# Optimization experiments

Measured on AMD Instinct MI355X. Metric: run time of the kernel, lower is better.

Reference implementation:

```python
import jax, jax.numpy as jnp
import numpy as np

K = 6                      # max_displacement / pad_size
WIN = 2 * K + 1            # displacement window side
D = WIN * WIN              # number of affinity channels (169)


def setup_inputs() -> dict:
    key = jax.random.key(0)
    k1, k2 = jax.random.split(key)
    aff = jax.random.normal(k1, (4, D, 192, 192), dtype=jnp.float32)
    input2 = jax.random.normal(k2, (4, 64, 192, 192), dtype=jnp.float32)
    return {"aff": aff, "input2": input2}


def reference(aff, input2):
    # output[b,c,y,x] = sum_{dy,dx in [-k,k]} aff[b, idx(dy,dx), y, x]
    #                   * input2_zeropad[b, c, y+dy, x+dx]
    # Scanned over the (2k+1)^2 displacements to avoid materializing the
    # [B, D, C, H, W] cost-volume intermediate.
    B, C, H, W = input2.shape
    Dn = aff.shape[1]
    win = int(round(Dn ** 0.5))
    k = (win - 1) // 2
    padded = jnp.pad(input2, ((0, 0), (0, 0), (k, k), (k, k)))  # [B,C,H+2k,W+2k]
    aff_t = jnp.transpose(aff, (1, 0, 2, 3))  # [D,B,H,W]
    ds = jnp.arange(Dn)

    def body(acc, xs):
        d, a = xs                      # a: [B,H,W]
        dy = d // win                  # 0..2k (offset into padded rows)
        dx = d % win                   # 0..2k (offset into padded cols)
        patch = jax.lax.dynamic_slice(padded, (0, 0, dy, dx), (B, C, H, W))
        return acc + a[:, None, :, :] * patch, None

    out, _ = jax.lax.scan(body, jnp.zeros_like(input2), (ds, aff_t))
    return out
```

## Files before the change

### kernel.cpp

```cpp
#include <hip/hip_runtime.h>


#define KD   6
#define WIN  13
#define ND   169
#define NB   4
#define NC   64
#define NH   192
#define NW   192
#define XH   96
#define PITCHW 68
#define NTH  192

typedef _Float16 half2v __attribute__((ext_vector_type(2)));

static __device__ __forceinline__ half2v h2(unsigned u) {
    return __builtin_bit_cast(half2v, u);
}
static __device__ __forceinline__ unsigned pk(float a, float b) {
    return __builtin_bit_cast(unsigned, __builtin_amdgcn_cvt_pkrtz(a, b));
}

#if __has_builtin(__builtin_amdgcn_fdot2)
#define FDOT2(a, b, c) __builtin_amdgcn_fdot2((a), (b), (c), false)
#else
static __device__ __forceinline__ float fdot2_fb(half2v a, half2v b, float c) {
    return fmaf((float)a.x, (float)b.x, fmaf((float)a.y, (float)b.y, c));
}
#define FDOT2(a, b, c) fdot2_fb((a), (b), (c))
#endif

__global__ __launch_bounds__(NTH)
__attribute__((amdgpu_waves_per_eu(2, 4)))
void mxassemble(const float* __restrict__ aff,
                const float* __restrict__ in2,
                float* __restrict__ out) {
    __shared__ unsigned ldsw[NC * PITCHW];

    const int y    = blockIdx.x;
    const int half = blockIdx.y;
    const int b    = blockIdx.z;
    const int t    = threadIdx.x;
    const int l    = t & 63;
    const int wv   = t >> 6;
    const int cg   = l & 7;
    const int xs   = l >> 3;
    const int X0   = half * XH;
    const int x0   = X0 + wv * 32 + xs * 4;

    {
        const int w0 = (half == 0) ? 0 : 52;
        for (int i = t; i < NC * 2; i += NTH) {
            const int c = i >> 1;
            const int q = i & 1;
            *(uint2*)&ldsw[c * PITCHW + w0 + 2 * q] = make_uint2(0u, 0u);
        }
    }

    float acc[8][4];
#pragma unroll
    for (int i = 0; i < 8; ++i)
#pragma unroll
        for (int j = 0; j < 4; ++j) acc[i][j] = 0.f;

    const float* in2_b = in2 + (size_t)b * NC * NH * NW;
    const float* aff_p = aff + (size_t)b * ND * NH * NW + (size_t)y * NW;

    for (int dy = 0; dy < WIN; ++dy) {
        const int r = y + dy - KD;
        const bool valid = (r >= 0) && (r < NH);

        __syncthreads();

        unsigned Ap[6][4];
        unsigned Al[4];
        if (valid) {
            const float* ap = aff_p + (size_t)(dy * WIN) * NH * NW + x0;
            float4 Af[13];
#pragma unroll
            for (int dx = 0; dx < WIN; ++dx)
                Af[dx] = *(const float4*)&ap[(size_t)dx * NH * NW];

            for (int ii = t; ii < NC * 28; ii += NTH) {
                const int c  = ii / 28;
                const int q  = ii - c * 28;
                const int xg = X0 - 8 + 4 * q;
                if (xg >= 0 && xg < NW) {
                    const float4 v =
                        *(const float4*)&in2_b[((size_t)c * NH + r) * NW + xg];
                    uint2 w;
                    w.x = pk(v.x, v.y);
                    w.y = pk(v.z, v.w);
                    *(uint2*)&ldsw[c * PITCHW + 2 * q] = w;
                }
            }

#pragma unroll
            for (int m = 0; m < 6; ++m) {
                Ap[m][0] = pk(Af[2*m].x, Af[2*m+1].x);
                Ap[m][1] = pk(Af[2*m].y, Af[2*m+1].y);
                Ap[m][2] = pk(Af[2*m].z, Af[2*m+1].z);
                Ap[m][3] = pk(Af[2*m].w, Af[2*m+1].w);
            }
            Al[0] = pk(Af[12].x, 0.f);
            Al[1] = pk(Af[12].y, 0.f);
            Al[2] = pk(Af[12].z, 0.f);
            Al[3] = pk(Af[12].w, 0.f);
        }
        __syncthreads();
        if (!valid) continue;

#pragma unroll
        for (int i = 0; i < 8; ++i) {
            const int c = cg + 8 * i;
            const unsigned* wp = &ldsw[c * PITCHW + ((x0 - X0) >> 1)];
            const uint2 t0 = *(const uint2*)&wp[0];
            const uint2 t1 = *(const uint2*)&wp[2];
            const uint2 t2 = *(const uint2*)&wp[4];
            const uint2 t3 = *(const uint2*)&wp[6];
            const uint2 t4 = *(const uint2*)&wp[8];
            const unsigned P1 = t0.y, P2 = t1.x, P3 = t1.y, P4 = t2.x;
            const unsigned P5 = t2.y, P6 = t3.x, P7 = t3.y, P8 = t4.x;
            const unsigned P9 = t4.y;
            const unsigned S1 = (P1 >> 16) | (P2 << 16);
            const unsigned S2 = (P2 >> 16) | (P3 << 16);
            const unsigned S3 = (P3 >> 16) | (P4 << 16);
            const unsigned S4 = (P4 >> 16) | (P5 << 16);
            const unsigned S5 = (P5 >> 16) | (P6 << 16);
            const unsigned S6 = (P6 >> 16) | (P7 << 16);
            const unsigned S7 = (P7 >> 16) | (P8 << 16);
            const unsigned S8 = (P8 >> 16) | (P9 << 16);

            float a0 = acc[i][0], a1 = acc[i][1], a2 = acc[i][2], a3 = acc[i][3];
            a0 = FDOT2(h2(Ap[0][0]), h2(P1), a0);
            a0 = FDOT2(h2(Ap[1][0]), h2(P2), a0);
            a0 = FDOT2(h2(Ap[2][0]), h2(P3), a0);
            a0 = FDOT2(h2(Ap[3][0]), h2(P4), a0);
            a0 = FDOT2(h2(Ap[4][0]), h2(P5), a0);
            a0 = FDOT2(h2(Ap[5][0]), h2(P6), a0);
            a0 = FDOT2(h2(Al[0]),    h2(P7), a0);
            a1 = FDOT2(h2(Ap[0][1]), h2(S1), a1);
            a1 = FDOT2(h2(Ap[1][1]), h2(S2), a1);
            a1 = FDOT2(h2(Ap[2][1]), h2(S3), a1);
            a1 = FDOT2(h2(Ap[3][1]), h2(S4), a1);
            a1 = FDOT2(h2(Ap[4][1]), h2(S5), a1);
            a1 = FDOT2(h2(Ap[5][1]), h2(S6), a1);
            a1 = FDOT2(h2(Al[1]),    h2(S7), a1);
            a2 = FDOT2(h2(Ap[0][2]), h2(P2), a2);
            a2 = FDOT2(h2(Ap[1][2]), h2(P3), a2);
            a2 = FDOT2(h2(Ap[2][2]), h2(P4), a2);
            a2 = FDOT2(h2(Ap[3][2]), h2(P5), a2);
            a2 = FDOT2(h2(Ap[4][2]), h2(P6), a2);
            a2 = FDOT2(h2(Ap[5][2]), h2(P7), a2);
            a2 = FDOT2(h2(Al[2]),    h2(P8), a2);
            a3 = FDOT2(h2(Ap[0][3]), h2(S2), a3);
            a3 = FDOT2(h2(Ap[1][3]), h2(S3), a3);
            a3 = FDOT2(h2(Ap[2][3]), h2(S4), a3);
            a3 = FDOT2(h2(Ap[3][3]), h2(S5), a3);
            a3 = FDOT2(h2(Ap[4][3]), h2(S6), a3);
            a3 = FDOT2(h2(Ap[5][3]), h2(S7), a3);
            a3 = FDOT2(h2(Al[3]),    h2(S8), a3);
            acc[i][0] = a0; acc[i][1] = a1; acc[i][2] = a2; acc[i][3] = a3;
        }
    }

    float* ob = out + (((size_t)(b * NC + cg) * NH) + y) * NW + x0;
#pragma unroll
    for (int i = 0; i < 8; ++i) {
        *(float4*)&ob[(size_t)(8 * i) * NH * NW] =
            make_float4(acc[i][0], acc[i][1], acc[i][2], acc[i][3]);
    }
}

extern "C" void kernel_launch(void* const* d_in, const int* in_sizes, int n_in,
                              void* d_out, int out_size, void* d_ws, size_t ws_size,
                              hipStream_t stream) {
    const float* aff = (const float*)d_in[0];
    const float* in2 = (const float*)d_in[1];
    float* outp = (float*)d_out;
    dim3 grid(NH, NW / XH, NB);
    dim3 block(NTH);
    hipLaunchKernelGGL(mxassemble, grid, block, 0, stream, aff, in2, outp);
}
```

Measured before the change: 308.3 us.

## Compute two output rows per block with double-buffered LDS row staging

Each block now produces two adjacent output rows over a 64-wide x tile. It streams 14 input rows through a double-buffered LDS and reuses each staged row for both output rows. Global loads for the next row and its affinity are issued before the current row's dot products, so load latency can overlap compute and there is one barrier per row. The grid is remapped with an interleaved block index, and the thread/channel split changes to 16 channel groups over 256 threads. Risks are higher register pressure from two accumulator sets and two packed-affinity sets, plus more halo traffic per output from the narrower tile.

```diff
diff --git a/kernel.cpp b/kernel.cpp
--- a/kernel.cpp
+++ b/kernel.cpp
@@ -8,9 +8,10 @@
 #define NC   64
 #define NH   192
 #define NW   192
-#define XH   96
-#define PITCHW 68
-#define NTH  192
+#define XH   64
+#define PITCHW 42
+#define BUFW (NC * PITCHW)
+#define NTH  256
 
 typedef _Float16 half2v __attribute__((ext_vector_type(2)));
 
@@ -30,145 +31,204 @@
 #define FDOT2(a, b, c) fdot2_fb((a), (b), (c))
 #endif
 
-__global__ __launch_bounds__(NTH)
-__attribute__((amdgpu_waves_per_eu(2, 4)))
+static __device__ __forceinline__ void aff_issue(const float* __restrict__ ap,
+                                                 float4 (&Af)[13]) {
+#pragma unroll
+    for (int dx = 0; dx < WIN; ++dx)
+        Af[dx] = *(const float4*)&ap[(size_t)dx * (NH * NW)];
+}
+
+static __device__ __forceinline__ void aff_pack(const float4 (&Af)[13],
+                                                unsigned (&P)[7][4]) {
+#pragma unroll
+    for (int m = 0; m < 6; ++m) {
+        P[m][0] = pk(Af[2*m].x, Af[2*m+1].x);
+        P[m][1] = pk(Af[2*m].y, Af[2*m+1].y);
+        P[m][2] = pk(Af[2*m].z, Af[2*m+1].z);
+        P[m][3] = pk(Af[2*m].w, Af[2*m+1].w);
+    }
+    P[6][0] = pk(Af[12].x, 0.f);
+    P[6][1] = pk(Af[12].y, 0.f);
+    P[6][2] = pk(Af[12].z, 0.f);
+    P[6][3] = pk(Af[12].w, 0.f);
+}
+
+static __device__ __forceinline__ void pass_y(const unsigned* __restrict__ wpb,
+                                              const unsigned (&P)[7][4],
+                                              float (&acc)[4][4]) {
+#pragma unroll
+    for (int i = 0; i < 4; ++i) {
+        const unsigned* wp = wpb + i * (16 * PITCHW);
+        const uint2 t0 = *(const uint2*)&wp[0];
+        const uint2 t1 = *(const uint2*)&wp[2];
+        const uint2 t2 = *(const uint2*)&wp[4];
+        const uint2 t3 = *(const uint2*)&wp[6];
+        const uint2 t4 = *(const uint2*)&wp[8];
+        const unsigned P1 = t0.y, P2 = t1.x, P3 = t1.y, P4 = t2.x;
+        const unsigned P5 = t2.y, P6 = t3.x, P7 = t3.y, P8 = t4.x;
+        const unsigned P9 = t4.y;
+        const unsigned S1 = (P1 >> 16) | (P2 << 16);
+        const unsigned S2 = (P2 >> 16) | (P3 << 16);
+        const unsigned S3 = (P3 >> 16) | (P4 << 16);
+        const unsigned S4 = (P4 >> 16) | (P5 << 16);
+        const unsigned S5 = (P5 >> 16) | (P6 << 16);
+        const unsigned S6 = (P6 >> 16) | (P7 << 16);
+        const unsigned S7 = (P7 >> 16) | (P8 << 16);
+        const unsigned S8 = (P8 >> 16) | (P9 << 16);
+
+        float a0 = acc[i][0], a1 = acc[i][1], a2 = acc[i][2], a3 = acc[i][3];
+        a0 = FDOT2(h2(P[0][0]), h2(P1), a0);
+        a0 = FDOT2(h2(P[1][0]), h2(P2), a0);
+        a0 = FDOT2(h2(P[2][0]), h2(P3), a0);
+        a0 = FDOT2(h2(P[3][0]), h2(P4), a0);
+        a0 = FDOT2(h2(P[4][0]), h2(P5), a0);
+        a0 = FDOT2(h2(P[5][0]), h2(P6), a0);
+        a0 = FDOT2(h2(P[6][0]), h2(P7), a0);
+        a1 = FDOT2(h2(P[0][1]), h2(S1), a1);
+        a1 = FDOT2(h2(P[1][1]), h2(S2), a1);
+        a1 = FDOT2(h2(P[2][1]), h2(S3), a1);
+        a1 = FDOT2(h2(P[3][1]), h2(S4), a1);
+        a1 = FDOT2(h2(P[4][1]), h2(S5), a1);
+        a1 = FDOT2(h2(P[5][1]), h2(S6), a1);
+        a1 = FDOT2(h2(P[6][1]), h2(S7), a1);
+        a2 = FDOT2(h2(P[0][2]), h2(P2), a2);
+        a2 = FDOT2(h2(P[1][2]), h2(P3), a2);
+        a2 = FDOT2(h2(P[2][2]), h2(P4), a2);
+        a2 = FDOT2(h2(P[3][2]), h2(P5), a2);
+        a2 = FDOT2(h2(P[4][2]), h2(P6), a2);
+        a2 = FDOT2(h2(P[5][2]), h2(P7), a2);
+        a2 = FDOT2(h2(P[6][2]), h2(P8), a2);
+        a3 = FDOT2(h2(P[0][3]), h2(S2), a3);
+        a3 = FDOT2(h2(P[1][3]), h2(S3), a3);
+        a3 = FDOT2(h2(P[2][3]), h2(S4), a3);
+        a3 = FDOT2(h2(P[3][3]), h2(S5), a3);
+        a3 = FDOT2(h2(P[4][3]), h2(S6), a3);
+        a3 = FDOT2(h2(P[5][3]), h2(S7), a3);
+        a3 = FDOT2(h2(P[6][3]), h2(S8), a3);
+        acc[i][0] = a0; acc[i][1] = a1; acc[i][2] = a2; acc[i][3] = a3;
+    }
+}
+
+__global__ __launch_bounds__(NTH, 2)
 void mxassemble(const float* __restrict__ aff,
                 const float* __restrict__ in2,
                 float* __restrict__ out) {
-    __shared__ unsigned ldsw[NC * PITCHW];
-
-    const int y    = blockIdx.x;
-    const int half = blockIdx.y;
-    const int b    = blockIdx.z;
+    __shared__ unsigned ldsw[2 * BUFW];
+
+    const int bx = blockIdx.x;
+    const int g  = bx & 7;
+    const int k  = bx >> 3;
+    const int b  = k / 12;
+    const int by = 12 * g + (k - 12 * b);
+    const int y0 = 2 * by;
+    const int xb = blockIdx.y;
+    const int X0 = xb * XH;
+
     const int t    = threadIdx.x;
     const int l    = t & 63;
     const int wv   = t >> 6;
-    const int cg   = l & 7;
-    const int xs   = l >> 3;
-    const int X0   = half * XH;
-    const int x0   = X0 + wv * 32 + xs * 4;
-
-    {
-        const int w0 = (half == 0) ? 0 : 52;
-        for (int i = t; i < NC * 2; i += NTH) {
-            const int c = i >> 1;
-            const int q = i & 1;
-            *(uint2*)&ldsw[c * PITCHW + w0 + 2 * q] = make_uint2(0u, 0u);
+    const int cg   = l & 15;
+    const int xs   = l >> 4;
+    const int slot = wv * 4 + xs;
+    const int x0   = X0 + slot * 4;
+
+    if (xb != 1) {
+        const int w0 = (xb == 0) ? 0 : 36;
+        if (t < NC * 2) {
+            const int c = t >> 1, qq = t & 1;
+            *(uint2*)&ldsw[c * PITCHW + w0 + 2 * qq]        = make_uint2(0u, 0u);
+            *(uint2*)&ldsw[BUFW + c * PITCHW + w0 + 2 * qq] = make_uint2(0u, 0u);
         }
     }
 
-    float acc[8][4];
-#pragma unroll
-    for (int i = 0; i < 8; ++i)
-#pragma unroll
-        for (int j = 0; j < 4; ++j) acc[i][j] = 0.f;
-
-    const float* in2_b = in2 + (size_t)b * NC * NH * NW;
-    const float* aff_p = aff + (size_t)b * ND * NH * NW + (size_t)y * NW;
-
-    for (int dy = 0; dy < WIN; ++dy) {
-        const int r = y + dy - KD;
-        const bool valid = (r >= 0) && (r < NH);
-
+    int wadr[5], goff[5];
+#pragma unroll
+    for (int s = 0; s < 5; ++s) {
+        const int ii = t + NTH * s;
+        const int c  = ii / 20;
+        const int q  = ii - 20 * c;
+        const int xg = X0 - 8 + 4 * q;
+        const bool ok = (xg >= 0) && (xg < NW);
+        wadr[s] = ok ? (c * PITCHW + 2 * q) : -1;
+        goff[s] = c * (NH * NW) + xg;
+    }
+
+    float acc0[4][4], acc1[4][4];
+#pragma unroll
+    for (int i = 0; i < 4; ++i)
+#pragma unroll
+        for (int j = 0; j < 4; ++j) { acc0[i][j] = 0.f; acc1[i][j] = 0.f; }
+
+    const float* in2_b  = in2 + (size_t)b * NC * NH * NW;
+    const float* aff_y0 = aff + (size_t)b * ND * NH * NW + (size_t)y0 * NW + x0;
+    const float* aff_y1 = aff_y0 + NW;
+    const int wbase = cg * PITCHW + 2 * slot;
+
+    float4 Af[13];
+    unsigned PA[7][4], PB[7][4];
+
+    aff_issue(aff_y0, Af);
+    if (y0 - KD >= 0) {
+        const float* p = in2_b + (size_t)(y0 - KD) * NW;
+        float4 Sv[5];
+#pragma unroll
+        for (int s = 0; s < 5; ++s)
+            if (wadr[s] >= 0) Sv[s] = *(const float4*)&p[goff[s]];
+#pragma unroll
+        for (int s = 0; s < 5; ++s)
+            if (wadr[s] >= 0) {
+                uint2 w; w.x = pk(Sv[s].x, Sv[s].y); w.y = pk(Sv[s].z, Sv[s].w);
+                *(uint2*)&ldsw[wadr[s]] = w;
+            }
+    }
+    aff_pack(Af, PA);
+    __syncthreads();
+
+    const float* apB = aff_y1;
+    const float* apA = aff_y0 + (size_t)(WIN * NH * NW);
+
+    for (int rr = 0; rr < 14; ++rr) {
+        const int r = y0 - KD + rr;
+        const bool rowvalid = (r >= 0) && (r < NH);
+        const int rn = r + 1;
+        const bool stage_next = (rr < 13) && (rn >= 0) && (rn < NH);
+        unsigned* curw = ldsw + ((rr & 1) ? BUFW : 0);
+        unsigned* nxtw = ldsw + ((rr & 1) ? 0 : BUFW);
+
+        if (rr < 13) aff_issue(apB, Af);
+        float4 Sv[5];
+        if (stage_next) {
+            const float* p = in2_b + (size_t)rn * NW;
+#pragma unroll
+            for (int s = 0; s < 5; ++s)
+                if (wadr[s] >= 0) Sv[s] = *(const float4*)&p[goff[s]];
+        }
+        if (rowvalid && rr >= 1) pass_y(curw + wbase, PB, acc1);
+        if (rr < 13) aff_pack(Af, PB);
+        if (stage_next) {
+#pragma unroll
+            for (int s = 0; s < 5; ++s)
+                if (wadr[s] >= 0) {
+                    uint2 w; w.x = pk(Sv[s].x, Sv[s].y); w.y = pk(Sv[s].z, Sv[s].w);
+                    *(uint2*)&nxtw[wadr[s]] = w;
+                }
+        }
+        if (rr < 12) aff_issue(apA, Af);
+        if (rowvalid && rr <= 12) pass_y(curw + wbase, PA, acc0);
+        if (rr < 12) aff_pack(Af, PA);
+
+        apB += (size_t)(WIN * NH * NW);
+        apA += (size_t)(WIN * NH * NW);
         __syncthreads();
-
-        unsigned Ap[6][4];
-        unsigned Al[4];
-        if (valid) {
-            const float* ap = aff_p + (size_t)(dy * WIN) * NH * NW + x0;
-            float4 Af[13];
-#pragma unroll
-            for (int dx = 0; dx < WIN; ++dx)
-                Af[dx] = *(const float4*)&ap[(size_t)dx * NH * NW];
-
-            for (int ii = t; ii < NC * 28; ii += NTH) {
-                const int c  = ii / 28;
-                const int q  = ii - c * 28;
-                const int xg = X0 - 8 + 4 * q;
-                if (xg >= 0 && xg < NW) {
-                    const float4 v =
-                        *(const float4*)&in2_b[((size_t)c * NH + r) * NW + xg];
-                    uint2 w;
-                    w.x = pk(v.x, v.y);
-                    w.y = pk(v.z, v.w);
-                    *(uint2*)&ldsw[c * PITCHW + 2 * q] = w;
-                }
-            }
-
-#pragma unroll
-            for (int m = 0; m < 6; ++m) {
-                Ap[m][0] = pk(Af[2*m].x, Af[2*m+1].x);
-                Ap[m][1] = pk(Af[2*m].y, Af[2*m+1].y);
-                Ap[m][2] = pk(Af[2*m].z, Af[2*m+1].z);
-                Ap[m][3] = pk(Af[2*m].w, Af[2*m+1].w);
-            }
-            Al[0] = pk(Af[12].x, 0.f);
-            Al[1] = pk(Af[12].y, 0.f);
-            Al[2] = pk(Af[12].z, 0.f);
-            Al[3] = pk(Af[12].w, 0.f);
-        }
-        __syncthreads();
-        if (!valid) continue;
-
-#pragma unroll
-        for (int i = 0; i < 8; ++i) {
-            const int c = cg + 8 * i;
-            const unsigned* wp = &ldsw[c * PITCHW + ((x0 - X0) >> 1)];
-            const uint2 t0 = *(const uint2*)&wp[0];
-            const uint2 t1 = *(const uint2*)&wp[2];
-            const uint2 t2 = *(const uint2*)&wp[4];
-            const uint2 t3 = *(const uint2*)&wp[6];
-            const uint2 t4 = *(const uint2*)&wp[8];
-            const unsigned P1 = t0.y, P2 = t1.x, P3 = t1.y, P4 = t2.x;
-            const unsigned P5 = t2.y, P6 = t3.x, P7 = t3.y, P8 = t4.x;
-            const unsigned P9 = t4.y;
-            const unsigned S1 = (P1 >> 16) | (P2 << 16);
-            const unsigned S2 = (P2 >> 16) | (P3 << 16);
-            const unsigned S3 = (P3 >> 16) | (P4 << 16);
-            const unsigned S4 = (P4 >> 16) | (P5 << 16);
-            const unsigned S5 = (P5 >> 16) | (P6 << 16);
-            const unsigned S6 = (P6 >> 16) | (P7 << 16);
-            const unsigned S7 = (P7 >> 16) | (P8 << 16);
-            const unsigned S8 = (P8 >> 16) | (P9 << 16);
-
-            float a0 = acc[i][0], a1 = acc[i][1], a2 = acc[i][2], a3 = acc[i][3];
-            a0 = FDOT2(h2(Ap[0][0]), h2(P1), a0);
-            a0 = FDOT2(h2(Ap[1][0]), h2(P2), a0);
-            a0 = FDOT2(h2(Ap[2][0]), h2(P3), a0);
-            a0 = FDOT2(h2(Ap[3][0]), h2(P4), a0);
-            a0 = FDOT2(h2(Ap[4][0]), h2(P5), a0);
-            a0 = FDOT2(h2(Ap[5][0]), h2(P6), a0);
-            a0 = FDOT2(h2(Al[0]),    h2(P7), a0);
-            a1 = FDOT2(h2(Ap[0][1]), h2(S1), a1);
-            a1 = FDOT2(h2(Ap[1][1]), h2(S2), a1);
-            a1 = FDOT2(h2(Ap[2][1]), h2(S3), a1);
-            a1 = FDOT2(h2(Ap[3][1]), h2(S4), a1);
-            a1 = FDOT2(h2(Ap[4][1]), h2(S5), a1);
-            a1 = FDOT2(h2(Ap[5][1]), h2(S6), a1);
-            a1 = FDOT2(h2(Al[1]),    h2(S7), a1);
-            a2 = FDOT2(h2(Ap[0][2]), h2(P2), a2);
-            a2 = FDOT2(h2(Ap[1][2]), h2(P3), a2);
-            a2 = FDOT2(h2(Ap[2][2]), h2(P4), a2);
-            a2 = FDOT2(h2(Ap[3][2]), h2(P5), a2);
-            a2 = FDOT2(h2(Ap[4][2]), h2(P6), a2);
-            a2 = FDOT2(h2(Ap[5][2]), h2(P7), a2);
-            a2 = FDOT2(h2(Al[2]),    h2(P8), a2);
-            a3 = FDOT2(h2(Ap[0][3]), h2(S2), a3);
-            a3 = FDOT2(h2(Ap[1][3]), h2(S3), a3);
-            a3 = FDOT2(h2(Ap[2][3]), h2(S4), a3);
-            a3 = FDOT2(h2(Ap[3][3]), h2(S5), a3);
-            a3 = FDOT2(h2(Ap[4][3]), h2(S6), a3);
-            a3 = FDOT2(h2(Ap[5][3]), h2(S7), a3);
-            a3 = FDOT2(h2(Al[3]),    h2(S8), a3);
-            acc[i][0] = a0; acc[i][1] = a1; acc[i][2] = a2; acc[i][3] = a3;
-        }
-    }
-
-    float* ob = out + (((size_t)(b * NC + cg) * NH) + y) * NW + x0;
-#pragma unroll
-    for (int i = 0; i < 8; ++i) {
-        *(float4*)&ob[(size_t)(8 * i) * NH * NW] =
-            make_float4(acc[i][0], acc[i][1], acc[i][2], acc[i][3]);
+    }
+
+    float* ob = out + (((size_t)b * NC + cg) * NH + y0) * NW + x0;
+#pragma unroll
+    for (int i = 0; i < 4; ++i) {
+        *(float4*)&ob[(size_t)(16 * i) * NH * NW] =
+            make_float4(acc0[i][0], acc0[i][1], acc0[i][2], acc0[i][3]);
+        *(float4*)&ob[(size_t)(16 * i) * NH * NW + NW] =
+            make_float4(acc1[i][0], acc1[i][1], acc1[i][2], acc1[i][3]);
     }
 }
 
@@ -178,7 +238,7 @@
     const float* aff = (const float*)d_in[0];
     const float* in2 = (const float*)d_in[1];
     float* outp = (float*)d_out;
-    dim3 grid(NH, NW / XH, NB);
+    dim3 grid(384, 3, 1);
     dim3 block(NTH);
     hipLaunchKernelGGL(mxassemble, grid, block, 0, stream, aff, in2, outp);
 }
```

Result: no change. 309.2 us (+0.3%).
